# Kernel tuning notes

Hardware: AMD Instinct MI355X
Metric: run time of the kernel (lower is better)

## Reference

```python
import jax, jax.numpy as jnp
import numpy as np
from jax import lax

B, C, HW = 128, 32, 16
N_E = 4096
PNS = (1, 2, 3, 4, 5, 6, 8, 10, 13, 16)
SN = len(PNS)
BETA, RESI = 0.25, 0.5
EPS = 1e-12

# PhiPartiallyShared tick schedule (K=4): which of the 4 Phi convs each scale uses
_TICKS = np.linspace(1.0 / 12.0, 1.0 - 1.0 / 12.0, 4)
PHI_IDX = [int(np.argmin(np.abs(_TICKS - si / (SN - 1)))) for si in range(SN)]


def _cubic_w(t, a=-0.75):
    # PyTorch bicubic kernel (a = -0.75)
    t = np.abs(t)
    return np.where(t <= 1.0, ((a + 2.0) * t - (a + 3.0)) * t * t + 1.0,
                    np.where(t < 2.0, (((t - 5.0) * t + 8.0) * t - 4.0) * a, 0.0))


def _bicubic_mat(n_in, n_out):
    # 1D resize matrix matching F.interpolate(mode='bicubic', align_corners=False)
    M = np.zeros((n_out, n_in), np.float32)
    scale = n_in / n_out
    for i in range(n_out):
        src = (i + 0.5) * scale - 0.5
        i0 = int(np.floor(src))
        f = src - i0
        for off in (-1, 0, 1, 2):
            w = float(_cubic_w(f - off))
            j = min(max(i0 + off, 0), n_in - 1)  # border replicate
            M[i, j] += w
    return M


def _area_mat(n_in, n_out):
    # 1D matrix matching F.interpolate(mode='area') == adaptive_avg_pool
    M = np.zeros((n_out, n_in), np.float32)
    for i in range(n_out):
        s = (i * n_in) // n_out
        e = -(-((i + 1) * n_in) // n_out)  # ceil
        M[i, s:e] = 1.0 / (e - s)
    return M


DOWN = {pn: jnp.asarray(_area_mat(HW, pn)) for pn in PNS[:-1]}
UP = {pn: jnp.asarray(_bicubic_mat(pn, HW)) for pn in PNS[:-1]}


def _resize2(x, M):
    # separable 2D resize: x [B,C,Y,X] -> [B,C,O,P]
    return jnp.einsum('oy,px,bcyx->bcop', M, M, x)


def _phi(h, w, b):
    conv = lax.conv_general_dilated(h, w, (1, 1), ((1, 1), (1, 1)),
                                    dimension_numbers=('NCHW', 'OIHW', 'NCHW'))
    conv = conv + b[None, :, None, None]
    return h * (1.0 - RESI) + conv * RESI


def _forward(f_input, codebook, phi_w, phi_b):
    f_ng = lax.stop_gradient(f_input)
    f_rest = f_ng
    f_hat = jnp.zeros_like(f_ng)
    cb_n = codebook / jnp.maximum(jnp.linalg.norm(codebook, axis=-1, keepdims=True), EPS)
    loss = jnp.asarray(0.0, jnp.float32)
    idx = None
    for si, pn in enumerate(PNS):
        x = _resize2(f_rest, DOWN[pn]) if si != SN - 1 else f_rest
        rest = x.transpose(0, 2, 3, 1).reshape(-1, C)          # [B*pn*pn, C]
        rest_n = rest / jnp.maximum(jnp.linalg.norm(rest, axis=-1, keepdims=True), EPS)
        idx = jnp.argmax(rest_n @ cb_n.T, axis=1)              # cosine-sim argmax
        h = codebook[idx].reshape(B, pn, pn, C).transpose(0, 3, 1, 2)
        if si != SN - 1:
            h = _resize2(h, UP[pn])
        k = PHI_IDX[si]
        h = _phi(h, phi_w[k], phi_b[k])
        f_hat = f_hat + h
        f_rest = f_rest - h
        loss = loss + BETA * jnp.mean((lax.stop_gradient(f_hat) - f_input) ** 2) \
                    + jnp.mean((f_hat - f_ng) ** 2)
    loss = loss / SN
    # straight-through estimator
    f_hat_st = f_input + lax.stop_gradient(f_hat - f_input)
    return f_hat_st, loss, idx


def setup_inputs() -> dict:
    key = jax.random.key(0)
    k1, k2, k3, k4 = jax.random.split(key, 4)
    return {
        'f_input': jax.random.normal(k1, (B, C, HW, HW), jnp.float32),
        'codebook': jax.random.normal(k2, (N_E, C), jnp.float32) * 0.5,
        'phi_w': jax.random.normal(k3, (4, C, C, 3, 3), jnp.float32) * (1.0 / np.sqrt(C * 9)),
        'phi_b': jax.random.normal(k4, (4, C), jnp.float32) * 0.01,
    }


def reference(f_input, codebook, phi_w, phi_b):
    f_hat, loss, idx = _forward(f_input, codebook, phi_w, phi_b)
    # perplexity of last-scale code usage
    n_tok = idx.shape[0]
    avg_probs = jnp.zeros((N_E,), jnp.float32).at[idx].add(1.0) / n_tok
    perplexity = jnp.exp(-jnp.sum(avg_probs * jnp.log(avg_probs + 1e-10)))
    return f_hat, loss, perplexity
```

## Files before the change

### kernel.cpp

```cpp
#include <hip/hip_runtime.h>
#include <stdint.h>
#include <math.h>


#define DEVI __device__ __forceinline__

static constexpr int NE = 4096;

typedef _Float16 half8 __attribute__((ext_vector_type(8)));
typedef float floatx4 __attribute__((ext_vector_type(4)));

DEVI int imax(int a, int b) { return a > b ? a : b; }

DEVI float dppL(float v) {
    return __int_as_float(
        __builtin_amdgcn_update_dpp(0, __float_as_int(v), 0x111, 0xF, 0xF, true));
}
DEVI float dppR(float v) {
    return __int_as_float(
        __builtin_amdgcn_update_dpp(0, __float_as_int(v), 0x101, 0xF, 0xF, true));
}

__global__ void __launch_bounds__(256) k_setup(const float* __restrict__ cb,
                                               const float* __restrict__ pw,
                                               _Float16* __restrict__ cbh,
                                               _Float16* __restrict__ cbl,
                                               float* __restrict__ wT,
                                               float* __restrict__ um,
                                               float* __restrict__ fhat,
                                               float* __restrict__ lossAcc) {
    int blk = blockIdx.x, tid = threadIdx.x;
    if (blk < 16) {
        int r = blk * 256 + tid;
        const float* src = cb + r * 32;
        float v[32];
        float ss = 0.f;
#pragma unroll
        for (int j = 0; j < 32; ++j) { v[j] = src[j]; ss += v[j] * v[j]; }
        float n = fmaxf(sqrtf(ss), 1e-12f);
#pragma unroll
        for (int j = 0; j < 32; ++j) {
            float x = v[j] / n;
            _Float16 h = (_Float16)x;
            cbh[r * 32 + j] = h;
            cbl[r * 32 + j] = (_Float16)(x - (float)h);
        }
    } else if (blk < 160) {
        int e = (blk - 16) * 256 + tid;
        int k = e / 9216, rem = e % 9216;
        int q8 = rem / 1152, rem2 = rem % 1152;
        int ic = rem2 / 36, r3 = rem2 % 36;
        int k9 = r3 / 4, o2 = r3 % 4;
        int oc = (q8 >> 2) * 16 + (q8 & 3) * 4 + o2;
        int ky = k9 / 3, kx = k9 % 3;
        wT[e] = pw[(((k * 32 + oc) * 32 + ic) * 3 + ky) * 3 + kx];
    } else if (blk == 160) {
        if (tid < 144) {
            const int pns[9] = {1, 2, 3, 4, 5, 6, 8, 10, 13};
            int si = tid / 16, y = tid % 16, pn = pns[si];
            double scale = (double)pn / 16.0;
            double src = ((double)y + 0.5) * scale - 0.5;
            double fl = floor(src);
            int i0 = (int)fl;
            double f = src - fl;
            float row[13];
            for (int j = 0; j < pn; ++j) row[j] = 0.f;
            const double a = -0.75;
#pragma unroll
            for (int off = -1; off <= 2; ++off) {
                double t2 = fabs(f - (double)off);
                double wgt;
                if (t2 <= 1.0)      wgt = ((a + 2.0) * t2 - (a + 3.0)) * t2 * t2 + 1.0;
                else if (t2 < 2.0)  wgt = (((t2 - 5.0) * t2 + 8.0) * t2 - 4.0) * a;
                else                wgt = 0.0;
                int j = i0 + off;
                j = j < 0 ? 0 : (j > pn - 1 ? pn - 1 : j);
                row[j] = (float)((double)row[j] + wgt);
            }
            for (int j = 0; j < pn; ++j) um[si * 256 + y * pn + j] = row[j];
        } else {
            for (int i = tid - 144; i < 4112; i += 112) ((int*)lossAcc)[i] = 0;
        }
    } else {
        int i = (blk - 161) * 1024 + tid * 4;
        float4 z = {0.f, 0.f, 0.f, 0.f};
        *(float4*)(fhat + i) = z;
    }
}


template <int PN>
__global__ void __launch_bounds__(256) k_down(const float* __restrict__ fin,
                                              const float* __restrict__ fhat,
                                              _Float16* __restrict__ xh,
                                              _Float16* __restrict__ xl) {
    constexpr int T = 128 * PN * PN;
    constexpr int Tp = ((T + 511) / 512) * 512;
    int id = blockIdx.x * 256 + threadIdx.x;
    if (id >= 32 * Tp) return;
    int t = id >> 5, c = id & 31;
    if (t >= T) { xh[id] = (_Float16)0.f; xl[id] = (_Float16)0.f; return; }
    int b = t / (PN * PN), r = t % (PN * PN), oy = r / PN, ox = r % PN;
    int sy = oy * 16 / PN, ey = ((oy + 1) * 16 + PN - 1) / PN;
    int sx = ox * 16 / PN, ex = ((ox + 1) * 16 + PN - 1) / PN;
    float wy = 1.f / (float)(ey - sy);
    float wx = 1.f / (float)(ex - sx);
    const float* pi = fin + b * 8192 + c * 256;
    const float* ph = fhat + b * 8192 + c * 256;
    float s = 0.f;
    if constexpr (PN == 1 || PN == 2 || PN == 4) {
        constexpr int W = 16 / PN;
        const float4* p4 = (const float4*)(pi + sy * 16 + sx);
        const float4* h4 = (const float4*)(ph + sy * 16 + sx);
#pragma unroll
        for (int y = 0; y < W; ++y)
#pragma unroll
            for (int xx = 0; xx < W / 4; ++xx) {
                float4 a = p4[y * 4 + xx], b4 = h4[y * 4 + xx];
                s += a.x - b4.x;
                s += a.y - b4.y;
                s += a.z - b4.z;
                s += a.w - b4.w;
            }
    } else {
        for (int y = sy; y < ey; ++y)
            for (int x = sx; x < ex; ++x)
                s += pi[y * 16 + x] - ph[y * 16 + x];
    }
    float v = s * (wy * wx);
    _Float16 h = (_Float16)v;
    xh[id] = h;
    xl[id] = (_Float16)(v - (float)h);
}

template <int PN, int SEG>
__global__ void __launch_bounds__(256, 2) k_quant(
        const half8* __restrict__ xh, const half8* __restrict__ xl,
        const half8* __restrict__ cbh8, const half8* __restrict__ cbl8,
        unsigned* __restrict__ bestp) {
    constexpr int T = 128 * PN * PN;
    constexpr int Tp = ((T + 511) / 512) * 512;
    constexpr int TB = Tp / 512;
    constexpr int CPS = 4096 / SEG;
    static_assert(CPS == 128, "reg-streamed sweep sized for CPS==128");

    int tid = threadIdx.x;
    int bt = blockIdx.x % TB, seg = blockIdx.x / TB;
    int wv = tid >> 6, lane = tid & 63;
    int n0 = lane & 15, g = lane >> 4;
    int tokbase = bt * 512 + wv * 128;
    int cbase = seg * CPS;

    half8 ah[8], al[8];
#pragma unroll
    for (int mt = 0; mt < 8; ++mt) {
        int tok = tokbase + mt * 16 + n0;
        ah[mt] = xh[tok * 4 + g];
        al[mt] = xl[tok * 4 + g];
    }

    int mx[8];
#pragma unroll
    for (int mt = 0; mt < 8; ++mt) mx[mt] = (int)0x80000000;

    const floatx4 z4 = {0.f, 0.f, 0.f, 0.f};
    const int KMASK = ~(CPS - 1);
    int lowg = CPS - 1 - g * 4;

    int code0 = cbase + n0;
    half8 bh = cbh8[code0 * 4 + g];
    half8 bl = cbl8[code0 * 4 + g];
#pragma unroll 1
    for (int nt = 0; nt < 8; ++nt) {
        int nn = (nt + 1) & 7;
        int codeN = cbase + nn * 16 + n0;
        half8 bhn = cbh8[codeN * 4 + g];
        half8 bln = cbl8[codeN * 4 + g];
        int lowb = lowg - nt * 16;
#pragma unroll
        for (int mt = 0; mt < 8; ++mt) {
            floatx4 c;
            c = __builtin_amdgcn_mfma_f32_16x16x32_f16(bh, ah[mt], z4, 0, 0, 0);
            c = __builtin_amdgcn_mfma_f32_16x16x32_f16(bl, ah[mt], c,  0, 0, 0);
            c = __builtin_amdgcn_mfma_f32_16x16x32_f16(bh, al[mt], c,  0, 0, 0);
            int k0 = (__float_as_int(c[0]) & KMASK) | (lowb - 0);
            int k1 = (__float_as_int(c[1]) & KMASK) | (lowb - 1);
            int k2 = (__float_as_int(c[2]) & KMASK) | (lowb - 2);
            int k3 = (__float_as_int(c[3]) & KMASK) | (lowb - 3);
            mx[mt] = imax(mx[mt], imax(k0, k1));
            mx[mt] = imax(mx[mt], imax(k2, k3));
        }
        bh = bhn;
        bl = bln;
    }

    unsigned* dst = bestp + (size_t)seg * Tp;
#pragma unroll
    for (int mt = 0; mt < 8; ++mt) {
        int k = mx[mt];
        k = imax(k, __shfl_xor(k, 16, 64));
        k = imax(k, __shfl_xor(k, 32, 64));
        if (g == (mt >> 1))
            dst[tokbase + mt * 16 + n0] = (unsigned)k;
    }
}

template <int PN, int SEG, int K, bool LAST>
__global__ void __launch_bounds__(512) k_upconv(
        const float* __restrict__ fin, float* __restrict__ fhat,
        const float* __restrict__ cbook,
        const unsigned* __restrict__ bestp,
        const float* __restrict__ wT, const float* __restrict__ phib,
        const float* __restrict__ um, float* __restrict__ lossAcc,
        int* __restrict__ hist, float* __restrict__ dout) {
    constexpr int NT = PN * PN;
    constexpr int T = 128 * NT;
    constexpr int Tp = ((T + 511) / 512) * 512;
    constexpr int CPS = 4096 / SEG;
    constexpr int RA = (PN < 16 && NT * 32 > 4096) ? NT * 32 : 4096;
    __shared__ __align__(16) float regionA[RA];
    __shared__ float hu1[(PN < 16) ? 32 * 6 * PN : 1];
    __shared__ float Us[(PN < 16) ? 16 * PN : 1];
    __shared__ int idxs[NT];
    __shared__ float red[8];
    float* S_hu = regionA;
    float* h0 = regionA;

    int img = blockIdx.x >> 2, q = blockIdx.x & 3;
    int y0 = q * 4;
    int tid = threadIdx.x;

    for (int e = tid; e < NT; e += 512) {
        int tok = img * NT + e;
        int k = (int)bestp[tok];
        int ws = 0;
#pragma unroll
        for (int s = 1; s < SEG; ++s) {
            int o = (int)bestp[(size_t)s * Tp + tok];
            bool gt = o > k;
            k = gt ? o : k;
            ws = gt ? s : ws;
        }
        idxs[e] = ws * CPS + (CPS - 1 - (k & (CPS - 1)));
    }
    if (PN < 16)
        for (int e = tid; e < 16 * PN; e += 512) Us[e] = um[e];
    __syncthreads();

    if (PN == 16) {
        if (LAST && tid < 64)
            atomicAdd(hist + idxs[y0 * 16 + tid], 1);
        for (int e = tid; e < 3072; e += 512) {
            int c = e / 96, r = e % 96;
            int rr = r >> 4, x = r & 15;
            int gy = y0 - 1 + rr;
            float v = 0.f;
            if (gy >= 0 && gy <= 15) v = cbook[idxs[gy * 16 + x] * 32 + c];
            S_hu[c * 128 + (rr + 1) * 16 + x] = v;
        }
    } else {
        for (int e = tid; e < NT * 32; e += 512) {
            int tk = e >> 5, c = e & 31;
            h0[e] = cbook[idxs[tk] * 32 + c];
        }
        __syncthreads();
        for (int e = tid; e < 6 * PN * 32; e += 512) {
            int c = e & 31, rest = e >> 5;
            int rr = rest / PN, i = rest % PN;
            int gy = y0 - 1 + rr;
            float s = 0.f;
            if (gy >= 0 && gy <= 15)
                for (int j = 0; j < PN; ++j)
                    s += Us[gy * PN + j] * h0[(j * PN + i) * 32 + c];
            hu1[(c * 6 + rr) * PN + i] = s;
        }
        __syncthreads();
        for (int e = tid; e < 3072; e += 512) {
            int c = e / 96, r = e % 96;
            int rr = r >> 4, x = r & 15;
            int gy = y0 - 1 + rr;
            float s = 0.f;
            if (gy >= 0 && gy <= 15)
                for (int i = 0; i < PN; ++i)
                    s += Us[x * PN + i] * hu1[(c * 6 + rr) * PN + i];
            S_hu[c * 128 + (rr + 1) * 16 + x] = s;
        }
    }
    __syncthreads();

    int px = tid & 63;
    int wvq = __builtin_amdgcn_readfirstlane(tid >> 6);
    int yo = px >> 4, x = px & 15;
    int y = y0 + yo;
    int ry = yo + 2;
    float acc[4] = {0.f, 0.f, 0.f, 0.f};
    const float* wk = wT + K * 9216 + wvq * 1152;
#pragma unroll 4
    for (int ic = 0; ic < 32; ++ic) {
        int a = ic * 128 + ry * 16 + x;
        float cm = S_hu[a - 16], cc = S_hu[a], cp = S_hu[a + 16];
        float lm = dppL(cm), lc = dppL(cc), lp = dppL(cp);
        float rm = dppR(cm), rc = dppR(cc), rp = dppR(cp);
        const float* w = wk + ic * 36;
#pragma unroll
        for (int o = 0; o < 4; ++o) {
            float s = acc[o];
            s = fmaf(w[o],      lm, s);
            s = fmaf(w[4 + o],  cm, s);
            s = fmaf(w[8 + o],  rm, s);
            s = fmaf(w[12 + o], lc, s);
            s = fmaf(w[16 + o], cc, s);
            s = fmaf(w[20 + o], rc, s);
            s = fmaf(w[24 + o], lp, s);
            s = fmaf(w[28 + o], cp, s);
            s = fmaf(w[32 + o], rp, s);
            acc[o] = s;
        }
    }

    float ss = 0.f;
    {
        int oc0 = (wvq >> 2) * 16 + (wvq & 3) * 4;
        int gbase = img * 8192 + oc0 * 256 + y * 16 + x;
        const float* bias = phib + K * 32 + oc0;
#pragma unroll
        for (int oi = 0; oi < 4; ++oi) {
            float conv = acc[oi] + bias[oi];
            float hval = 0.5f * S_hu[(oc0 + oi) * 128 + ry * 16 + x] + 0.5f * conv;
            float fh = fhat[gbase + oi * 256] + hval;
            fhat[gbase + oi * 256] = fh;
            if (LAST) dout[gbase + oi * 256] = fh;
            float d = fh - fin[gbase + oi * 256];
            ss = fmaf(d, d, ss);
        }
    }
    int lane = tid & 63;
#pragma unroll
    for (int m = 1; m < 64; m <<= 1) ss += __shfl_xor(ss, m, 64);
    if (lane == 0) red[tid >> 6] = ss;
    __syncthreads();
    if (tid == 0)
        atomicAdd(lossAcc, red[0] + red[1] + red[2] + red[3] +
                           red[4] + red[5] + red[6] + red[7]);
}

__global__ void __launch_bounds__(256) k_final(const float* __restrict__ lossAcc,
                                               const int* __restrict__ hist,
                                               float* __restrict__ out) {
    __shared__ float red[256];
    int tid = threadIdx.x;
    float s = 0.f;
    for (int i = tid; i < 4096; i += 256) {
        float p = (float)hist[i] * (1.f / 32768.f);
        s += p * logf(p + 1e-10f);
    }
    red[tid] = s;
    __syncthreads();
    for (int k = 128; k > 0; k >>= 1) {
        if (tid < k) red[tid] += red[tid + k];
        __syncthreads();
    }
    if (tid == 0) {
        out[1048577] = expf(-red[0]);
        float L = 0.f;
        for (int si = 0; si < 10; ++si) L += lossAcc[si];
        out[1048576] = L * 1.25f / 1048576.f * 0.1f;
    }
}


extern "C" void kernel_launch(void* const* d_in, const int* in_sizes, int n_in,
                              void* d_out, int out_size, void* d_ws, size_t ws_size,
                              hipStream_t stream) {
    const float* f_in  = (const float*)d_in[0];
    const float* cbook = (const float*)d_in[1];
    const float* phiw  = (const float*)d_in[2];
    const float* phib  = (const float*)d_in[3];
    float* out = (float*)d_out;
    char* base = (char*)d_ws;

    float* fhat    = (float*)(base);
    float* lossAcc = (float*)(base + 4194304);
    int*   hist    = (int*)  (base + 4194368);
    float* wT      = (float*)(base + 4210752);
    float* um      = (float*)(base + 4358208);
    _Float16* cbh  = (_Float16*)(base + 4367424);
    _Float16* cbl  = (_Float16*)(base + 4629568);
    _Float16* xh   = (_Float16*)(base + 4891712);
    _Float16* xl   = (_Float16*)(base + 6988864);
    unsigned* bestp = (unsigned*)(base + 9086016);

    k_setup<<<1185, 256, 0, stream>>>(cbook, phiw, cbh, cbl, wT, um, fhat, lossAcc);

#define SCALE(SI, PN, K, LAST)                                                         \
    {                                                                                  \
        constexpr int T = 128 * PN * PN;                                               \
        constexpr int Tp = ((T + 511) / 512) * 512;                                    \
        constexpr int TB = Tp / 512;                                                   \
        k_down<PN><<<(Tp * 32) / 256, 256, 0, stream>>>(f_in, fhat, xh, xl);           \
        k_quant<PN, 32><<<TB * 32, 256, 0, stream>>>(                                  \
            (const half8*)xh, (const half8*)xl, (const half8*)cbh,                     \
            (const half8*)cbl, bestp);                                                 \
        k_upconv<PN, 32, K, LAST><<<512, 512, 0, stream>>>(                            \
            f_in, fhat, cbook, bestp, wT, phib, um + SI * 256, lossAcc + SI, hist,     \
            out);                                                                      \
    }
    SCALE(0, 1, 0, false);
    SCALE(1, 2, 0, false);
    SCALE(2, 3, 0, false);
    SCALE(3, 4, 1, false);
    SCALE(4, 5, 1, false);
    SCALE(5, 6, 2, false);
    SCALE(6, 8, 2, false);
    SCALE(7, 10, 2, false);
    SCALE(8, 13, 3, false);
    SCALE(9, 16, 3, true);
#undef SCALE
    k_final<<<1, 256, 0, stream>>>(lossAcc, hist, out);
}
```

Before: 515.5 us.

## Stage residual tiles in shared memory for downsample; skip fhat zero-init

The downsample kernel now gives each block half of one image's channels (16 channels x 256 pixels). It loads fin-fhat into shared memory once with coalesced float4 reads, then computes every area-pooled token from LDS. Before, each thread re-read global memory with strided per-channel access. The fhat zero-fill in setup is removed, and a FIRST template flag makes the first scale treat fhat as zero in both downsample and upconv. Padding tokens are zeroed by one extra block. The risk is lower parallelism: only 256 blocks each do serial pooling loops for large PN.

```diff
diff --git a/kernel.cpp b/kernel.cpp
--- a/kernel.cpp
+++ b/kernel.cpp
@@ -27,7 +27,6 @@
                                                _Float16* __restrict__ cbl,
                                                float* __restrict__ wT,
                                                float* __restrict__ um,
-                                               float* __restrict__ fhat,
                                                float* __restrict__ lossAcc) {
     int blk = blockIdx.x, tid = threadIdx.x;
     if (blk < 16) {
@@ -54,7 +53,7 @@
         int oc = (q8 >> 2) * 16 + (q8 & 3) * 4 + o2;
         int ky = k9 / 3, kx = k9 % 3;
         wT[e] = pw[(((k * 32 + oc) * 32 + ic) * 3 + ky) * 3 + kx];
-    } else if (blk == 160) {
+    } else {
         if (tid < 144) {
             const int pns[9] = {1, 2, 3, 4, 5, 6, 8, 10, 13};
             int si = tid / 16, y = tid % 16, pn = pns[si];
@@ -81,56 +80,61 @@
         } else {
             for (int i = tid - 144; i < 4112; i += 112) ((int*)lossAcc)[i] = 0;
         }
-    } else {
-        int i = (blk - 161) * 1024 + tid * 4;
-        float4 z = {0.f, 0.f, 0.f, 0.f};
-        *(float4*)(fhat + i) = z;
-    }
-}
-
-
-template <int PN>
+    }
+}
+
+
+template <int PN, bool FIRST>
 __global__ void __launch_bounds__(256) k_down(const float* __restrict__ fin,
                                               const float* __restrict__ fhat,
                                               _Float16* __restrict__ xh,
                                               _Float16* __restrict__ xl) {
-    constexpr int T = 128 * PN * PN;
+    constexpr int NT = PN * PN;
+    constexpr int T = 128 * NT;
     constexpr int Tp = ((T + 511) / 512) * 512;
-    int id = blockIdx.x * 256 + threadIdx.x;
-    if (id >= 32 * Tp) return;
-    int t = id >> 5, c = id & 31;
-    if (t >= T) { xh[id] = (_Float16)0.f; xl[id] = (_Float16)0.f; return; }
-    int b = t / (PN * PN), r = t % (PN * PN), oy = r / PN, ox = r % PN;
-    int sy = oy * 16 / PN, ey = ((oy + 1) * 16 + PN - 1) / PN;
-    int sx = ox * 16 / PN, ex = ((ox + 1) * 16 + PN - 1) / PN;
-    float wy = 1.f / (float)(ey - sy);
-    float wx = 1.f / (float)(ex - sx);
-    const float* pi = fin + b * 8192 + c * 256;
-    const float* ph = fhat + b * 8192 + c * 256;
-    float s = 0.f;
-    if constexpr (PN == 1 || PN == 2 || PN == 4) {
-        constexpr int W = 16 / PN;
-        const float4* p4 = (const float4*)(pi + sy * 16 + sx);
-        const float4* h4 = (const float4*)(ph + sy * 16 + sx);
-#pragma unroll
-        for (int y = 0; y < W; ++y)
-#pragma unroll
-            for (int xx = 0; xx < W / 4; ++xx) {
-                float4 a = p4[y * 4 + xx], b4 = h4[y * 4 + xx];
-                s += a.x - b4.x;
-                s += a.y - b4.y;
-                s += a.z - b4.z;
-                s += a.w - b4.w;
-            }
-    } else {
+    int tid = threadIdx.x;
+    if (blockIdx.x >= 256) {
+        for (int i = tid; i < (Tp - T) * 32; i += 256) {
+            xh[T * 32 + i] = (_Float16)0.f;
+            xl[T * 32 + i] = (_Float16)0.f;
+        }
+        return;
+    }
+    __shared__ float r[16][260];
+    int img = blockIdx.x >> 1, ch = (blockIdx.x & 1) * 16;
+
+    const float4* pi4 = (const float4*)(fin + img * 8192 + ch * 256);
+    const float4* ph4 = (const float4*)(fhat + img * 8192 + ch * 256);
+    for (int i = tid; i < 1024; i += 256) {
+        float4 a = pi4[i];
+        float4 b;
+        if constexpr (FIRST) { b.x = 0.f; b.y = 0.f; b.z = 0.f; b.w = 0.f; }
+        else                 { b = ph4[i]; }
+        int c = i >> 6, p = (i & 63) * 4;
+        r[c][p]     = a.x - b.x;
+        r[c][p + 1] = a.y - b.y;
+        r[c][p + 2] = a.z - b.z;
+        r[c][p + 3] = a.w - b.w;
+    }
+    __syncthreads();
+
+    for (int e = tid; e < NT * 16; e += 256) {
+        int lt = e >> 4, cp = e & 15;
+        int oy = lt / PN, ox = lt % PN;
+        int sy = oy * 16 / PN, ey = ((oy + 1) * 16 + PN - 1) / PN;
+        int sx = ox * 16 / PN, ex = ((ox + 1) * 16 + PN - 1) / PN;
+        float wy = 1.f / (float)(ey - sy);
+        float wx = 1.f / (float)(ex - sx);
+        float s = 0.f;
         for (int y = sy; y < ey; ++y)
             for (int x = sx; x < ex; ++x)
-                s += pi[y * 16 + x] - ph[y * 16 + x];
-    }
-    float v = s * (wy * wx);
-    _Float16 h = (_Float16)v;
-    xh[id] = h;
-    xl[id] = (_Float16)(v - (float)h);
+                s += r[cp][y * 16 + x];
+        float v = s * (wy * wx);
+        _Float16 h = (_Float16)v;
+        int gid = (img * NT + lt) * 32 + ch + cp;
+        xh[gid] = h;
+        xl[gid] = (_Float16)(v - (float)h);
+    }
 }
 
 template <int PN, int SEG>
@@ -205,7 +209,7 @@
     }
 }
 
-template <int PN, int SEG, int K, bool LAST>
+template <int PN, int SEG, int K, bool FIRST, bool LAST>
 __global__ void __launch_bounds__(512) k_upconv(
         const float* __restrict__ fin, float* __restrict__ fhat,
         const float* __restrict__ cbook,
@@ -327,7 +331,7 @@
         for (int oi = 0; oi < 4; ++oi) {
             float conv = acc[oi] + bias[oi];
             float hval = 0.5f * S_hu[(oc0 + oi) * 128 + ry * 16 + x] + 0.5f * conv;
-            float fh = fhat[gbase + oi * 256] + hval;
+            float fh = (FIRST ? 0.f : fhat[gbase + oi * 256]) + hval;
             fhat[gbase + oi * 256] = fh;
             if (LAST) dout[gbase + oi * 256] = fh;
             float d = fh - fin[gbase + oi * 256];
@@ -390,31 +394,32 @@
     _Float16* xl   = (_Float16*)(base + 6988864);
     unsigned* bestp = (unsigned*)(base + 9086016);
 
-    k_setup<<<1185, 256, 0, stream>>>(cbook, phiw, cbh, cbl, wT, um, fhat, lossAcc);
-
-#define SCALE(SI, PN, K, LAST)                                                         \
+    k_setup<<<161, 256, 0, stream>>>(cbook, phiw, cbh, cbl, wT, um, lossAcc);
+
+#define SCALE(SI, PN, K, FIRST, LAST)                                                  \
     {                                                                                  \
         constexpr int T = 128 * PN * PN;                                               \
         constexpr int Tp = ((T + 511) / 512) * 512;                                    \
         constexpr int TB = Tp / 512;                                                   \
-        k_down<PN><<<(Tp * 32) / 256, 256, 0, stream>>>(f_in, fhat, xh, xl);           \
+        constexpr int PADB = (Tp > T) ? 1 : 0;                                         \
+        k_down<PN, FIRST><<<256 + PADB, 256, 0, stream>>>(f_in, fhat, xh, xl);         \
         k_quant<PN, 32><<<TB * 32, 256, 0, stream>>>(                                  \
             (const half8*)xh, (const half8*)xl, (const half8*)cbh,                     \
             (const half8*)cbl, bestp);                                                 \
-        k_upconv<PN, 32, K, LAST><<<512, 512, 0, stream>>>(                            \
+        k_upconv<PN, 32, K, FIRST, LAST><<<512, 512, 0, stream>>>(                     \
             f_in, fhat, cbook, bestp, wT, phib, um + SI * 256, lossAcc + SI, hist,     \
             out);                                                                      \
     }
-    SCALE(0, 1, 0, false);
-    SCALE(1, 2, 0, false);
-    SCALE(2, 3, 0, false);
-    SCALE(3, 4, 1, false);
-    SCALE(4, 5, 1, false);
-    SCALE(5, 6, 2, false);
-    SCALE(6, 8, 2, false);
-    SCALE(7, 10, 2, false);
-    SCALE(8, 13, 3, false);
-    SCALE(9, 16, 3, true);
+    SCALE(0, 1, 0, true, false);
+    SCALE(1, 2, 0, false, false);
+    SCALE(2, 3, 0, false, false);
+    SCALE(3, 4, 1, false, false);
+    SCALE(4, 5, 1, false, false);
+    SCALE(5, 6, 2, false, false);
+    SCALE(6, 8, 2, false, false);
+    SCALE(7, 10, 2, false, false);
+    SCALE(8, 13, 3, false, false);
+    SCALE(9, 16, 3, false, true);
 #undef SCALE
     k_final<<<1, 256, 0, stream>>>(lossAcc, hist, out);
 }
```

Result: faster. 465.9 us (-9.6%).
